# Optimization experiments

Hardware: AMD Instinct MI355X
Metric: run time of the kernel (lower is better)

Reference implementation:

```python
import jax, jax.numpy as jnp
import numpy as np

F_DIM = 256; L = 4; B = 1; H = 160; W = 160; FH = 1024; N = B * H * W

def _ln(x, w, b):
    mu = jnp.mean(x, -1, keepdims=True)
    var = jnp.mean(jnp.square(x - mu), -1, keepdims=True)
    return (x - mu) * jax.lax.rsqrt(var + 1e-5) * w + b

def _conv(x, w, b, groups=1, pad=0):
    y = jax.lax.conv_general_dilated(x, w, (1, 1), [(pad, pad), (pad, pad)],
                                     dimension_numbers=('NCHW', 'OIHW', 'NCHW'),
                                     feature_group_count=groups)
    return y + b[None, :, None, None]

def _wsilu(x):
    return jax.nn.sigmoid(4.0 * x) * x

def setup_inputs() -> dict:
    key = jax.random.key(0)
    ks = iter(jax.random.split(key, 40))
    nk = lambda: next(ks)
    s = 1.0 / np.sqrt(F_DIM).astype(np.float32)
    inp = {}
    inp['x'] = jax.random.normal(nk(), (B, 1, H, W), jnp.float32)
    inp['cin_w1'] = jax.random.normal(nk(), (F_DIM, 1, 1, 1), jnp.float32)
    inp['cin_b1'] = jnp.zeros((F_DIM,), jnp.float32)
    inp['cin_w2'] = jax.random.normal(nk(), (F_DIM, 1, 7, 7), jnp.float32) * 0.15
    inp['cin_b2'] = jnp.zeros((F_DIM,), jnp.float32)
    inp['ln0_w'] = jnp.ones((F_DIM,), jnp.float32); inp['ln0_b'] = jnp.zeros((F_DIM,), jnp.float32)
    inp['ln1_w'] = jnp.ones((L, F_DIM), jnp.float32); inp['ln1_b'] = jnp.zeros((L, F_DIM), jnp.float32)
    inp['ln2_w'] = jnp.ones((L, F_DIM), jnp.float32); inp['ln2_b'] = jnp.zeros((L, F_DIM), jnp.float32)
    for n in ['att_tmk', 'att_tmv', 'att_tmr', 'ffn_tmk', 'ffn_tmr']:
        inp[n] = jax.random.uniform(nk(), (L, F_DIM), jnp.float32)
    inp['att_tf'] = jax.random.normal(nk(), (L, F_DIM), jnp.float32) * 0.5
    # time_decay is stored as -exp(raw) by the module's loader
    inp['att_td'] = -jnp.exp(jax.random.normal(nk(), (L, F_DIM), jnp.float32) * 0.5)
    for n in ['att_kw', 'att_vw', 'att_rw', 'att_ow', 'ffn_rw']:
        inp[n] = jax.random.normal(nk(), (L, F_DIM, F_DIM), jnp.float32) * s
    inp['ffn_kw'] = jax.random.normal(nk(), (L, FH, F_DIM), jnp.float32) * s
    inp['ffn_vw'] = jax.random.normal(nk(), (L, F_DIM, FH), jnp.float32) * (1.0 / np.sqrt(FH).astype(np.float32))
    inp['spa_dw_w'] = jax.random.normal(nk(), (L, F_DIM, 1, 7, 7), jnp.float32) * 0.15
    inp['spa_dw_b'] = jnp.zeros((L, F_DIM), jnp.float32)
    inp['spa_pw_w'] = jax.random.normal(nk(), (L, F_DIM, F_DIM, 1, 1), jnp.float32) * s
    inp['spa_pw_b'] = jnp.zeros((L, F_DIM), jnp.float32)
    st = jnp.zeros((5 * L, N, F_DIM), jnp.float32)
    st = st.at[4::5].add(-1e30)  # pp slots start at -1e30 as in torch init
    inp['state0'] = st
    return inp

def reference(x, cin_w1, cin_b1, cin_w2, cin_b2, ln0_w, ln0_b, ln1_w, ln1_b,
              ln2_w, ln2_b, att_tmk, att_tmv, att_tmr, att_tf, att_td,
              att_kw, att_vw, att_rw, att_ow, ffn_tmk, ffn_tmr, ffn_kw,
              ffn_vw, ffn_rw, spa_dw_w, spa_dw_b, spa_pw_w, spa_pw_b, state0):
    # conv stem: 1x1 -> depthwise 7x7 -> WSiLU
    d = _conv(x, cin_w1, cin_b1)
    d = _wsilu(_conv(d, cin_w2, cin_b2, groups=F_DIM, pad=3))
    d = d.transpose(0, 2, 3, 1).reshape(N, F_DIM)  # 'b f h w -> (b h w) f'
    for i in range(L):
        if i == 0:
            d = _ln(d, ln0_w, ln0_b)
        # --- SA: single-step RWKV WKV ---
        xs = _ln(d, ln1_w[i], ln1_b[i])
        sp = state0[5 * i + 1]
        aa = state0[5 * i + 2]; bb = state0[5 * i + 3]; pp = state0[5 * i + 4]
        xk = xs * att_tmk[i] + sp * (1 - att_tmk[i])
        xv = xs * att_tmv[i] + sp * (1 - att_tmv[i])
        xr = xs * att_tmr[i] + sp * (1 - att_tmr[i])
        r = jax.nn.sigmoid(xr @ att_rw[i].T)
        k = xk @ att_kw[i].T
        v = xv @ att_vw[i].T
        ww = att_tf[i] + k
        p = jnp.maximum(pp, ww)
        e1 = jnp.exp(pp - p); e2 = jnp.exp(ww - p)
        wkv = (e1 * aa + e2 * v) / (e1 * bb + e2)
        d = d + (r * wkv) @ att_ow[i].T
        # --- FF: squared-relu channel mix ---
        xs = _ln(d, ln2_w[i], ln2_b[i])
        sp = state0[5 * i + 0]
        xk = xs * ffn_tmk[i] + sp * (1 - ffn_tmk[i])
        xr = xs * ffn_tmr[i] + sp * (1 - ffn_tmr[i])
        rr = jax.nn.sigmoid(xr @ ffn_rw[i].T)
        kk = jnp.square(jax.nn.relu(xk @ ffn_kw[i].T))
        d = d + rr * (kk @ ffn_vw[i].T)
        # --- spatial residual block ---
        img = d.reshape(B, H, W, F_DIM).transpose(0, 3, 1, 2)
        img = img + _conv(_conv(img, spa_dw_w[i], spa_dw_b[i], groups=F_DIM, pad=3),
                          spa_pw_w[i], spa_pw_b[i])
        d = img.transpose(0, 2, 3, 1).reshape(N, F_DIM)
    return d.reshape(B, H, W, F_DIM).transpose(0, 3, 1, 2)
```

## Files before the change

### kernel.cpp

```cpp
#include <hip/hip_runtime.h>
#include <hip/hip_bf16.h>
#include <cstdint>
#include <cstddef>

#define F_DIMC 256
#define FHC    1024
#define IMGH   160
#define IMGW   160
#define NTOK   25600
#define NLAY   4

using bf16 = __hip_bfloat16;
using f16  = _Float16;
typedef __attribute__((ext_vector_type(8))) short bf16x8;
typedef __attribute__((ext_vector_type(4))) float f32x4;

#define MFMA16(a, b, c) __builtin_amdgcn_mfma_f32_16x16x32_bf16((a), (b), (c), 0, 0, 0)

union H4 { f16 h[4]; uint2 u; };
union Pack4 { bf16 h[4]; uint2 u; };
union Pack8 { bf16 h[8]; bf16x8 v; };

__global__ void prep_k(const float* __restrict__ kw, const float* __restrict__ vw,
                       const float* __restrict__ rw, const float* __restrict__ tmk,
                       const float* __restrict__ tmv, const float* __restrict__ tmr,
                       const float* __restrict__ fkw, const float* __restrict__ ftmk,
                       const float* __restrict__ frw, const float* __restrict__ ftmr,
                       const float* __restrict__ ow, const float* __restrict__ pw,
                       const float* __restrict__ fvw, const float* __restrict__ dww,
                       bf16* __restrict__ Wcat, bf16* __restrict__ fkw2,
                       bf16* __restrict__ frw2, bf16* __restrict__ owb,
                       bf16* __restrict__ pwb, bf16* __restrict__ fvwb,
                       float* __restrict__ dwT)
{
    int z = blockIdx.y;
    int idx = blockIdx.x * 256 + threadIdx.x;
    if (z < 4) {
        int l = z;
        int c = idx & 511, cc = c & 255;
        bool hi2 = c >= 256;
        int r = idx >> 9;
        if (r < 768) {
            const float* W; const float* T; int rr = r;
            if (r < 256)      { W = kw; T = tmk; }
            else if (r < 512) { W = vw; T = tmv; rr = r - 256; }
            else              { W = rw; T = tmr; rr = r - 512; }
            float w = W[(size_t)l * 65536 + rr * 256 + cc];
            float t = T[l * 256 + cc];
            Wcat[(size_t)l * 768 * 512 + (size_t)r * 512 + c] = __float2bfloat16(w * (hi2 ? 1.f - t : t));
        } else if (r < 1792) {
            int rr = r - 768;
            float w = fkw[(size_t)l * 1024 * 256 + rr * 256 + cc];
            float t = ftmk[l * 256 + cc];
            fkw2[(size_t)l * 1024 * 512 + (size_t)rr * 512 + c] = __float2bfloat16(w * (hi2 ? 1.f - t : t));
        } else {
            int rr = r - 1792;
            float w = frw[(size_t)l * 65536 + rr * 256 + cc];
            float t = ftmr[l * 256 + cc];
            frw2[(size_t)l * 256 * 512 + (size_t)rr * 512 + c] = __float2bfloat16(w * (hi2 ? 1.f - t : t));
        }
    } else {
        int q = z - 4;
        if (q == 0)      { if (idx < 262144)  owb[idx]  = __float2bfloat16(ow[idx]); }
        else if (q == 1) { if (idx < 262144)  pwb[idx]  = __float2bfloat16(pw[idx]); }
        else if (q == 2) { if (idx < 1048576) fvwb[idx] = __float2bfloat16(fvw[idx]); }
        else {
            if (idx < 50176) {
                int f = idx & 255; int lt = idx >> 8; int t = lt % 49; int l = lt / 49;
                dwT[idx] = dww[((size_t)l * F_DIMC + f) * 49 + t];
            }
        }
    }
}

__global__ __launch_bounds__(256)
void stem2_k(const float* __restrict__ x, const float* __restrict__ w1,
             const float* __restrict__ b1, const float* __restrict__ w2,
             const float* __restrict__ b2, f16* __restrict__ d)
{
    __shared__ float wts[49][64];
    __shared__ float w1s[64], b1s[64], b2s[64];
    __shared__ float2 xp[7][22];
    const int tid = threadIdx.x;
    const int f0 = blockIdx.y * 64;
    const int y = blockIdx.x / 10;
    const int x0 = (blockIdx.x % 10) * 16;

    for (int idx = tid; idx < 49 * 64; idx += 256) {
        int t = idx >> 6, fl = idx & 63;
        wts[t][fl] = w2[(f0 + fl) * 49 + t];
    }
    if (tid < 64) {
        w1s[tid] = w1[f0 + tid];
        b1s[tid] = b1[f0 + tid];
        b2s[tid] = b2[f0 + tid];
    }
    for (int p = tid; p < 7 * 22; p += 256) {
        int py = p / 22, px = p % 22;
        int gy = y + py - 3, gx = x0 + px - 3;
        bool ok = (unsigned)gy < IMGH && (unsigned)gx < IMGW;
        xp[py][px] = ok ? make_float2(x[gy * IMGW + gx], 1.f) : make_float2(0.f, 0.f);
    }
    __syncthreads();

    const int fl = tid & 63;
    const int xbase = (tid >> 6) * 4;
    float acc[4] = {0.f, 0.f, 0.f, 0.f}, accw[4] = {0.f, 0.f, 0.f, 0.f};
    #pragma unroll
    for (int ky = 0; ky < 7; ++ky) {
        float2 row[10];
        #pragma unroll
        for (int q = 0; q < 10; ++q) row[q] = xp[ky][xbase + q];
        #pragma unroll
        for (int kx = 0; kx < 7; ++kx) {
            float w = wts[ky * 7 + kx][fl];
            #pragma unroll
            for (int j = 0; j < 4; ++j) {
                acc[j]  = fmaf(row[j + kx].x, w, acc[j]);
                accw[j] = fmaf(row[j + kx].y, w, accw[j]);
            }
        }
    }
    const float w1f = w1s[fl], b1f = b1s[fl], b2f = b2s[fl];
    #pragma unroll
    for (int j = 0; j < 4; ++j) {
        float u = fmaf(w1f, acc[j], fmaf(b1f, accw[j], b2f));
        int pix = y * IMGW + x0 + xbase + j;
        d[(size_t)pix * F_DIMC + f0 + fl] = (f16)(u / (1.f + __expf(-4.f * u)));
    }
}

__device__ __forceinline__ void wave_ln(float* x, const float* __restrict__ w,
                                        const float* __restrict__ b, int lane)
{
    float s = x[0] + x[1] + x[2] + x[3];
    #pragma unroll
    for (int m = 1; m < 64; m <<= 1) s += __shfl_xor(s, m, 64);
    float mu = s * 0.00390625f;
    float t0 = x[0] - mu, t1 = x[1] - mu, t2 = x[2] - mu, t3 = x[3] - mu;
    float v = t0 * t0 + t1 * t1 + t2 * t2 + t3 * t3;
    #pragma unroll
    for (int m = 1; m < 64; m <<= 1) v += __shfl_xor(v, m, 64);
    float inv = rsqrtf(v * 0.00390625f + 1e-5f);
    f32x4 wv = *(const f32x4*)(w + lane * 4);
    f32x4 bv = *(const f32x4*)(b + lane * 4);
    x[0] = t0 * inv * wv[0] + bv[0];
    x[1] = t1 * inv * wv[1] + bv[1];
    x[2] = t2 * inv * wv[2] + bv[2];
    x[3] = t3 * inv * wv[3] + bv[3];
}

__global__ __launch_bounds__(256)
void ln_first_k(f16* __restrict__ d, const float* __restrict__ ln0w,
                const float* __restrict__ ln0b, const float* __restrict__ l1w,
                const float* __restrict__ l1b, bf16* __restrict__ xs)
{
    const int lane = threadIdx.x & 63;
    const int n = blockIdx.x * 4 + (threadIdx.x >> 6);
    const int base = n * F_DIMC + lane * 4;
    H4 hv; hv.u = *(const uint2*)(d + base);
    float xo[4] = {(float)hv.h[0], (float)hv.h[1], (float)hv.h[2], (float)hv.h[3]};
    wave_ln(xo, ln0w, ln0b, lane);
    H4 o;
    #pragma unroll
    for (int j = 0; j < 4; ++j) o.h[j] = (f16)xo[j];
    *(uint2*)(d + base) = o.u;
    wave_ln(xo, l1w, l1b, lane);
    Pack4 p;
    #pragma unroll
    for (int j = 0; j < 4; ++j) p.h[j] = __float2bfloat16(xo[j]);
    *(uint2*)(xs + base) = p.u;
}

__device__ __forceinline__ void stage_swz16(const bf16* __restrict__ g, int lda,
                                            bf16* lds, int tid)
{
    #pragma unroll
    for (int s = 0; s < 8; ++s) {
        int chunk = s * 256 + tid;
        int row = chunk >> 4, c16 = chunk & 15;
        int gc = c16 ^ (row & 15);
        __builtin_amdgcn_global_load_lds(
            (const __attribute__((address_space(1))) void*)(g + (size_t)row * lda + gc * 8),
            (__attribute__((address_space(3))) void*)(lds + chunk * 8), 16, 0, 0);
    }
}
__device__ __forceinline__ void stage_f32_swz16(const float* __restrict__ g, int lda,
                                                bf16* lds, int tid)
{
    #pragma unroll
    for (int s = 0; s < 8; ++s) {
        int chunk = s * 256 + tid;
        int row = chunk >> 4, c16 = chunk & 15;
        int gc = c16 ^ (row & 15);
        const float* src = g + (size_t)row * lda + gc * 8;
        f32x4 a = *(const f32x4*)src;
        f32x4 b = *(const f32x4*)(src + 4);
        Pack8 p;
        #pragma unroll
        for (int j = 0; j < 4; ++j) p.h[j] = __float2bfloat16(a[j]);
        #pragma unroll
        for (int j = 0; j < 4; ++j) p.h[4 + j] = __float2bfloat16(b[j]);
        *(bf16x8*)(lds + chunk * 8) = p.v;
    }
}
__device__ __forceinline__ void stage_swz8(const bf16* __restrict__ g, int lda,
                                           bf16* lds, int tid, int nloads)
{
    #pragma unroll
    for (int s = 0; s < 8; ++s) {
        if (s >= nloads) break;
        int chunk = s * 256 + tid;
        int row = chunk >> 3, c = chunk & 7;
        int gc = c ^ (row & 7);
        __builtin_amdgcn_global_load_lds(
            (const __attribute__((address_space(1))) void*)(g + (size_t)row * lda + gc * 8),
            (__attribute__((address_space(3))) void*)(lds + chunk * 8), 16, 0, 0);
    }
}

template<int RB>
__device__ __forceinline__ bf16x8 frag_ld(const bf16* lds, int row, int cb)
{
    constexpr int M = (RB >= 256) ? 15 : (RB / 16 - 1);
    return *(const bf16x8*)((const char*)lds + row * RB + (cb ^ ((row & M) << 4)));
}

template<int EPI>
__global__ __launch_bounds__(256, 2)
void gemm128_k(const bf16* __restrict__ A1, const float* __restrict__ A2f,
               const bf16* __restrict__ Bw, int Nout,
               f16* __restrict__ Cf, bf16* __restrict__ Cb)
{
    __shared__ __align__(16) bf16 As[128 * 128];
    __shared__ __align__(16) bf16 Bs[128 * 128];
    const int tid = threadIdx.x, lane = tid & 63, wave = tid >> 6;
    const int wr = wave >> 1, wc = wave & 1;
    const int lr = lane & 15, hi = lane >> 4;
    const int m0 = blockIdx.x * 128, n0 = blockIdx.y * 128;

    f32x4 acc[4][4];
    #pragma unroll
    for (int m = 0; m < 4; ++m)
        #pragma unroll
        for (int n = 0; n < 4; ++n) acc[m][n] = (f32x4){0.f, 0.f, 0.f, 0.f};

    #pragma unroll
    for (int kt = 0; kt < 512; kt += 128) {
        if (kt < 256)
            stage_swz16(A1 + (size_t)m0 * 256 + kt, 256, As, tid);
        else
            stage_f32_swz16(A2f + (size_t)m0 * 256 + (kt - 256), 256, As, tid);
        stage_swz16(Bw + (size_t)n0 * 512 + kt, 512, Bs, tid);
        __syncthreads();
        #pragma unroll
        for (int ks = 0; ks < 4; ++ks) {
            int cb = ks * 64 + hi * 16;
            bf16x8 a[4], b[4];
            #pragma unroll
            for (int mf = 0; mf < 4; ++mf) a[mf] = frag_ld<256>(As, wr * 64 + mf * 16 + lr, cb);
            #pragma unroll
            for (int nf = 0; nf < 4; ++nf) b[nf] = frag_ld<256>(Bs, wc * 64 + nf * 16 + lr, cb);
            #pragma unroll
            for (int mf = 0; mf < 4; ++mf)
                #pragma unroll
                for (int nf = 0; nf < 4; ++nf)
                    acc[mf][nf] = MFMA16(a[mf], b[nf], acc[mf][nf]);
        }
        __syncthreads();
    }

    const int lr0 = hi * 4;
    #pragma unroll
    for (int mf = 0; mf < 4; ++mf)
        #pragma unroll
        for (int nf = 0; nf < 4; ++nf) {
            int col = n0 + wc * 64 + nf * 16 + lr;
            #pragma unroll
            for (int j = 0; j < 4; ++j) {
                int row = m0 + wr * 64 + mf * 16 + lr0 + j;
                size_t cidx = (size_t)row * Nout + col;
                float v = acc[mf][nf][j];
                if constexpr (EPI == 0) Cf[cidx] = (f16)v;
                else { float t = fmaxf(v, 0.f); Cb[cidx] = __float2bfloat16(t * t); }
            }
        }
}

__global__ __launch_bounds__(256, 2)
void gemmow_k(const f16* __restrict__ G, const float* __restrict__ aa,
              const float* __restrict__ bb, const float* __restrict__ pp,
              const float* __restrict__ tf, const bf16* __restrict__ W,
              f16* __restrict__ d, bf16* __restrict__ xs,
              const float* __restrict__ lnw, const float* __restrict__ lnb)
{
    __shared__ __align__(16) bf16 As[64 * 256];
    __shared__ __align__(16) bf16 Bs[256 * 64];
    __shared__ float2 lnp[64][4];
    const int tid = threadIdx.x, lane = tid & 63, wave = tid >> 6;
    const int lr = lane & 15, hi = lane >> 4;
    const int m0 = blockIdx.x * 64;

    stage_swz8(W, 256, Bs, tid, 8);

    #pragma unroll
    for (int rb = 0; rb < 4; ++rb) {
        int r = rb * 16 + (tid >> 4);
        int row = m0 + r;
        const f16* g = G + (size_t)row * 768;
        const size_t sb = (size_t)row * F_DIMC;
        #pragma unroll
        for (int j = 0; j < 4; ++j) {
            int c = (tid & 15) * 4 + j * 64;
            H4 k4; k4.u = *(const uint2*)(g + c);
            H4 v4; v4.u = *(const uint2*)(g + 256 + c);
            H4 r4; r4.u = *(const uint2*)(g + 512 + c);
            f32x4 a4 = *(const f32x4*)(aa + sb + c);
            f32x4 b4 = *(const f32x4*)(bb + sb + c);
            f32x4 p4 = *(const f32x4*)(pp + sb + c);
            f32x4 t4 = *(const f32x4*)(tf + c);
            Pack4 po;
            #pragma unroll
            for (int q = 0; q < 4; ++q) {
                float ww = t4[q] + (float)k4.h[q];
                float p = fmaxf(p4[q], ww);
                float e1 = __expf(p4[q] - p);
                float e2 = __expf(ww - p);
                float wkv = (e1 * a4[q] + e2 * (float)v4.h[q]) / (e1 * b4[q] + e2);
                float rs = 1.f / (1.f + __expf(-(float)r4.h[q]));
                po.h[q] = __float2bfloat16(rs * wkv);
            }
            int chunk = c >> 3;
            int off = (c & 4) ? 8 : 0;
            *(uint2*)((char*)As + r * 512 + ((chunk ^ (r & 15)) << 4) + off) = po.u;
        }
    }
    __syncthreads();

    f32x4 acc[4][4];
    #pragma unroll
    for (int m = 0; m < 4; ++m)
        #pragma unroll
        for (int n = 0; n < 4; ++n) acc[m][n] = (f32x4){0.f, 0.f, 0.f, 0.f};

    #pragma unroll
    for (int kt = 0; kt < 256; kt += 64) {
        if (kt > 0) {
            stage_swz8(W + kt, 256, Bs, tid, 8);
            __syncthreads();
        }
        #pragma unroll
        for (int ks = 0; ks < 2; ++ks) {
            int cbA = kt * 2 + ks * 64 + hi * 16;
            int cbB = ks * 64 + hi * 16;
            bf16x8 a[4], b[4];
            #pragma unroll
            for (int mf = 0; mf < 4; ++mf) a[mf] = frag_ld<512>(As, mf * 16 + lr, cbA);
            #pragma unroll
            for (int nf = 0; nf < 4; ++nf) b[nf] = frag_ld<128>(Bs, wave * 64 + nf * 16 + lr, cbB);
            #pragma unroll
            for (int mf = 0; mf < 4; ++mf)
                #pragma unroll
                for (int nf = 0; nf < 4; ++nf)
                    acc[mf][nf] = MFMA16(a[mf], b[nf], acc[mf][nf]);
        }
        __syncthreads();
    }

    const int lr0 = hi * 4;
    #pragma unroll
    for (int mf = 0; mf < 4; ++mf) {
        #pragma unroll
        for (int j = 0; j < 4; ++j) {
            int row = m0 + mf * 16 + lr0 + j;
            float s = 0.f, q = 0.f;
            #pragma unroll
            for (int nf = 0; nf < 4; ++nf) {
                int col = wave * 64 + nf * 16 + lr;
                size_t ci = (size_t)row * F_DIMC + col;
                float v = acc[mf][nf][j] + (float)d[ci];
                acc[mf][nf][j] = v;
                d[ci] = (f16)v;
                s += v; q += v * v;
            }
            #pragma unroll
            for (int m = 1; m < 16; m <<= 1) {
                s += __shfl_xor(s, m, 64);
                q += __shfl_xor(q, m, 64);
            }
            if (lr == 0) lnp[mf * 16 + lr0 + j][wave] = make_float2(s, q);
        }
    }
    __syncthreads();
    #pragma unroll
    for (int mf = 0; mf < 4; ++mf) {
        #pragma unroll
        for (int j = 0; j < 4; ++j) {
            int ri = mf * 16 + lr0 + j;
            float S = 0.f, Q = 0.f;
            #pragma unroll
            for (int w2 = 0; w2 < 4; ++w2) {
                float2 p = lnp[ri][w2];
                S += p.x; Q += p.y;
            }
            float mu = S * 0.00390625f;
            float var = Q * 0.00390625f - mu * mu;
            float inv = rsqrtf(var + 1e-5f);
            int row = m0 + ri;
            #pragma unroll
            for (int nf = 0; nf < 4; ++nf) {
                int col = wave * 64 + nf * 16 + lr;
                float v = (acc[mf][nf][j] - mu) * inv * lnw[col] + lnb[col];
                xs[(size_t)row * F_DIMC + col] = __float2bfloat16(v);
            }
        }
    }
}

template<bool DOLN>
__global__ __launch_bounds__(256, 2)
void gemmpw_k(const bf16* __restrict__ A, const bf16* __restrict__ W,
              f16* __restrict__ d, bf16* __restrict__ xs,
              const float* __restrict__ lnw, const float* __restrict__ lnb,
              const float* __restrict__ bias)
{
    __shared__ __align__(16) bf16 As[64 * 64];
    __shared__ __align__(16) bf16 Bs[256 * 64];
    __shared__ float2 lnp[64][4];
    const int tid = threadIdx.x, lane = tid & 63, wave = tid >> 6;
    const int lr = lane & 15, hi = lane >> 4;
    const int m0 = blockIdx.x * 64;

    f32x4 acc[4][4];
    #pragma unroll
    for (int m = 0; m < 4; ++m)
        #pragma unroll
        for (int n = 0; n < 4; ++n) acc[m][n] = (f32x4){0.f, 0.f, 0.f, 0.f};

    #pragma unroll
    for (int kt = 0; kt < 256; kt += 64) {
        stage_swz8(A + (size_t)m0 * 256 + kt, 256, As, tid, 2);
        stage_swz8(W + kt, 256, Bs, tid, 8);
        __syncthreads();
        #pragma unroll
        for (int ks = 0; ks < 2; ++ks) {
            int cb = ks * 64 + hi * 16;
            bf16x8 a[4], b[4];
            #pragma unroll
            for (int mf = 0; mf < 4; ++mf) a[mf] = frag_ld<128>(As, mf * 16 + lr, cb);
            #pragma unroll
            for (int nf = 0; nf < 4; ++nf) b[nf] = frag_ld<128>(Bs, wave * 64 + nf * 16 + lr, cb);
            #pragma unroll
            for (int mf = 0; mf < 4; ++mf)
                #pragma unroll
                for (int nf = 0; nf < 4; ++nf)
                    acc[mf][nf] = MFMA16(a[mf], b[nf], acc[mf][nf]);
        }
        __syncthreads();
    }

    const int lr0 = hi * 4;
    #pragma unroll
    for (int mf = 0; mf < 4; ++mf) {
        #pragma unroll
        for (int j = 0; j < 4; ++j) {
            int row = m0 + mf * 16 + lr0 + j;
            float s = 0.f, q = 0.f;
            #pragma unroll
            for (int nf = 0; nf < 4; ++nf) {
                int col = wave * 64 + nf * 16 + lr;
                size_t ci = (size_t)row * F_DIMC + col;
                float v = acc[mf][nf][j] + (float)d[ci] + bias[col];
                acc[mf][nf][j] = v;
                d[ci] = (f16)v;
                s += v; q += v * v;
            }
            if constexpr (DOLN) {
                #pragma unroll
                for (int m = 1; m < 16; m <<= 1) {
                    s += __shfl_xor(s, m, 64);
                    q += __shfl_xor(q, m, 64);
                }
                if (lr == 0) lnp[mf * 16 + lr0 + j][wave] = make_float2(s, q);
            }
        }
    }
    if constexpr (DOLN) {
        __syncthreads();
        #pragma unroll
        for (int mf = 0; mf < 4; ++mf) {
            #pragma unroll
            for (int j = 0; j < 4; ++j) {
                int ri = mf * 16 + lr0 + j;
                float S = 0.f, Q = 0.f;
                #pragma unroll
                for (int w2 = 0; w2 < 4; ++w2) {
                    float2 p = lnp[ri][w2];
                    S += p.x; Q += p.y;
                }
                float mu = S * 0.00390625f;
                float var = Q * 0.00390625f - mu * mu;
                float inv = rsqrtf(var + 1e-5f);
                int row = m0 + ri;
                #pragma unroll
                for (int nf = 0; nf < 4; ++nf) {
                    int col = wave * 64 + nf * 16 + lr;
                    float v = (acc[mf][nf][j] - mu) * inv * lnw[col] + lnb[col];
                    xs[(size_t)row * F_DIMC + col] = __float2bfloat16(v);
                }
            }
        }
    }
}

__global__ __launch_bounds__(256, 2)
void fvwrr_k(const bf16* __restrict__ kkb, const bf16* __restrict__ fvw,
             const bf16* __restrict__ xs, const float* __restrict__ spf,
             const bf16* __restrict__ frw2, f16* __restrict__ d)
{
    __shared__ __align__(16) bf16 As[128 * 128];
    __shared__ __align__(16) bf16 Bs[128 * 128];
    const int tid = threadIdx.x, lane = tid & 63, wave = tid >> 6;
    const int wr = wave >> 1, wc = wave & 1;
    const int lr = lane & 15, hi = lane >> 4;
    const int m0 = blockIdx.x * 128, n0 = blockIdx.y * 128;

    f32x4 arr[4][4], am[4][4];
    #pragma unroll
    for (int m = 0; m < 4; ++m)
        #pragma unroll
        for (int n = 0; n < 4; ++n) {
            arr[m][n] = (f32x4){0.f, 0.f, 0.f, 0.f};
            am[m][n]  = (f32x4){0.f, 0.f, 0.f, 0.f};
        }

    #pragma unroll
    for (int kt = 0; kt < 512; kt += 128) {
        if (kt < 256)
            stage_swz16(xs + (size_t)m0 * 256 + kt, 256, As, tid);
        else
            stage_f32_swz16(spf + (size_t)m0 * 256 + (kt - 256), 256, As, tid);
        stage_swz16(frw2 + (size_t)n0 * 512 + kt, 512, Bs, tid);
        __syncthreads();
        #pragma unroll
        for (int ks = 0; ks < 4; ++ks) {
            int cb = ks * 64 + hi * 16;
            bf16x8 a[4], b[4];
            #pragma unroll
            for (int mf = 0; mf < 4; ++mf) a[mf] = frag_ld<256>(As, wr * 64 + mf * 16 + lr, cb);
            #pragma unroll
            for (int nf = 0; nf < 4; ++nf) b[nf] = frag_ld<256>(Bs, wc * 64 + nf * 16 + lr, cb);
            #pragma unroll
            for (int mf = 0; mf < 4; ++mf)
                #pragma unroll
                for (int nf = 0; nf < 4; ++nf)
                    arr[mf][nf] = MFMA16(a[mf], b[nf], arr[mf][nf]);
        }
        __syncthreads();
    }
    #pragma unroll
    for (int kt = 0; kt < 1024; kt += 128) {
        stage_swz16(kkb + (size_t)m0 * 1024 + kt, 1024, As, tid);
        stage_swz16(fvw + (size_t)n0 * 1024 + kt, 1024, Bs, tid);
        __syncthreads();
        #pragma unroll
        for (int ks = 0; ks < 4; ++ks) {
            int cb = ks * 64 + hi * 16;
            bf16x8 a[4], b[4];
            #pragma unroll
            for (int mf = 0; mf < 4; ++mf) a[mf] = frag_ld<256>(As, wr * 64 + mf * 16 + lr, cb);
            #pragma unroll
            for (int nf = 0; nf < 4; ++nf) b[nf] = frag_ld<256>(Bs, wc * 64 + nf * 16 + lr, cb);
            #pragma unroll
            for (int mf = 0; mf < 4; ++mf)
                #pragma unroll
                for (int nf = 0; nf < 4; ++nf)
                    am[mf][nf] = MFMA16(a[mf], b[nf], am[mf][nf]);
        }
        __syncthreads();
    }

    const int lr0 = hi * 4;
    #pragma unroll
    for (int mf = 0; mf < 4; ++mf)
        #pragma unroll
        for (int nf = 0; nf < 4; ++nf) {
            int col = n0 + wc * 64 + nf * 16 + lr;
            #pragma unroll
            for (int j = 0; j < 4; ++j) {
                int row = m0 + wr * 64 + mf * 16 + lr0 + j;
                size_t cidx = (size_t)row * F_DIMC + col;
                float rr = 1.f / (1.f + __expf(-arr[mf][nf][j]));
                d[cidx] = (f16)((float)d[cidx] + rr * am[mf][nf][j]);
            }
        }
}

__global__ __launch_bounds__(256)
void dwconv2_k(const f16* __restrict__ d, const float* __restrict__ wT,
               const float* __restrict__ bias, bf16* __restrict__ out)
{
    __shared__ float patch[196][64];
    __shared__ float wt[49][64];
    const int lane = threadIdx.x;
    const int ty = threadIdx.y;
    const int f0 = blockIdx.z * 64;
    const int w0 = blockIdx.x * 8, h0 = blockIdx.y * 8;

    for (int t = ty; t < 49; t += 4) wt[t][lane] = wT[t * F_DIMC + f0 + lane];
    for (int p = ty; p < 196; p += 4) {
        int py = p / 14, px = p % 14;
        int gy = h0 + py - 3, gx = w0 + px - 3;
        float v = 0.f;
        if ((unsigned)gy < IMGH && (unsigned)gx < IMGW)
            v = (float)d[(size_t)(gy * IMGW + gx) * F_DIMC + f0 + lane];
        patch[p][lane] = v;
    }
    __syncthreads();

    const float b = bias[f0 + lane];
    #pragma unroll
    for (int rr = 0; rr < 2; ++rr) {
        int ry = ty * 2 + rr;
        float acc8[8];
        #pragma unroll
        for (int px = 0; px < 8; ++px) acc8[px] = b;
        #pragma unroll
        for (int ky = 0; ky < 7; ++ky) {
            float rowv[14];
            #pragma unroll
            for (int c = 0; c < 14; ++c) rowv[c] = patch[(ry + ky) * 14 + c][lane];
            #pragma unroll
            for (int kx = 0; kx < 7; ++kx) {
                float w = wt[ky * 7 + kx][lane];
                #pragma unroll
                for (int px = 0; px < 8; ++px)
                    acc8[px] = fmaf(rowv[px + kx], w, acc8[px]);
            }
        }
        #pragma unroll
        for (int px = 0; px < 8; ++px)
            out[(size_t)((h0 + ry) * IMGW + (w0 + px)) * F_DIMC + f0 + lane] = __float2bfloat16(acc8[px]);
    }
}

__global__ __launch_bounds__(256)
void transpose_out_k(const f16* __restrict__ d, float* __restrict__ out)
{
    __shared__ float tile[32][33];
    const int n0 = blockIdx.x * 32, f0 = blockIdx.y * 32;
    const int tx = threadIdx.x, ty = threadIdx.y;
    for (int r = ty; r < 32; r += 8) tile[r][tx] = (float)d[(size_t)(n0 + r) * F_DIMC + f0 + tx];
    __syncthreads();
    for (int r = ty; r < 32; r += 8) out[(size_t)(f0 + r) * NTOK + n0 + tx] = tile[tx][r];
}

extern "C" void kernel_launch(void* const* d_in, const int* in_sizes, int n_in,
                              void* d_out, int out_size, void* d_ws, size_t ws_size,
                              hipStream_t stream)
{
    if (n_in < 30) return;
    const float* x        = (const float*)d_in[0];
    const float* cin_w1   = (const float*)d_in[1];
    const float* cin_b1   = (const float*)d_in[2];
    const float* cin_w2   = (const float*)d_in[3];
    const float* cin_b2   = (const float*)d_in[4];
    const float* ln0_w    = (const float*)d_in[5];
    const float* ln0_b    = (const float*)d_in[6];
    const float* ln1_w    = (const float*)d_in[7];
    const float* ln1_b    = (const float*)d_in[8];
    const float* ln2_w    = (const float*)d_in[9];
    const float* ln2_b    = (const float*)d_in[10];
    const float* att_tmk  = (const float*)d_in[11];
    const float* att_tmv  = (const float*)d_in[12];
    const float* att_tmr  = (const float*)d_in[13];
    const float* ffn_tmk  = (const float*)d_in[14];
    const float* ffn_tmr  = (const float*)d_in[15];
    const float* att_tf   = (const float*)d_in[16];
    const float* att_kw   = (const float*)d_in[18];
    const float* att_vw   = (const float*)d_in[19];
    const float* att_rw   = (const float*)d_in[20];
    const float* att_ow   = (const float*)d_in[21];
    const float* ffn_rw   = (const float*)d_in[22];
    const float* ffn_kw   = (const float*)d_in[23];
    const float* ffn_vw   = (const float*)d_in[24];
    const float* spa_dw_w = (const float*)d_in[25];
    const float* spa_dw_b = (const float*)d_in[26];
    const float* spa_pw_w = (const float*)d_in[27];
    const float* spa_pw_b = (const float*)d_in[28];
    const float* state0   = (const float*)d_in[29];
    float* out = (float*)d_out;

    const size_t NF = (size_t)NTOK * F_DIMC;
    char* wsp = (char*)d_ws;
    size_t off = 0;
    auto alloc = [&](size_t bytes) -> void* {
        void* p = wsp + off;
        off += (bytes + 255) & ~(size_t)255;
        return p;
    };
    f16*   d_buf = (f16*)alloc(NF * 2);
    bf16*  xs    = (bf16*)alloc(NF * 2);
    f16*   G     = (f16*)alloc((size_t)NTOK * 768 * 2);
    bf16*  ab    = (bf16*)alloc(NF * 2);
    bf16*  kkb   = (bf16*)alloc((size_t)NTOK * FHC * 2);
    bf16*  Wcat  = (bf16*)alloc((size_t)NLAY * 768 * 512 * 2);
    bf16*  fkw2  = (bf16*)alloc((size_t)NLAY * 1024 * 512 * 2);
    bf16*  frw2  = (bf16*)alloc((size_t)NLAY * 256 * 512 * 2);
    bf16*  owb   = (bf16*)alloc((size_t)NLAY * 65536 * 2);
    bf16*  pwb   = (bf16*)alloc((size_t)NLAY * 65536 * 2);
    bf16*  fvwb  = (bf16*)alloc((size_t)NLAY * 262144 * 2);
    float* dwT   = (float*)alloc((size_t)NLAY * 49 * F_DIMC * 4);
    if (off > ws_size) return;

    prep_k<<<dim3(4096, 8), dim3(256), 0, stream>>>(
        att_kw, att_vw, att_rw, att_tmk, att_tmv, att_tmr,
        ffn_kw, ffn_tmk, ffn_rw, ffn_tmr,
        att_ow, spa_pw_w, ffn_vw, spa_dw_w,
        Wcat, fkw2, frw2, owb, pwb, fvwb, dwT);

    stem2_k<<<dim3(IMGH * 10, 4), dim3(256), 0, stream>>>(x, cin_w1, cin_b1, cin_w2, cin_b2, d_buf);
    ln_first_k<<<dim3(NTOK / 4), dim3(256), 0, stream>>>(d_buf, ln0_w, ln0_b, ln1_w, ln1_b, xs);

    for (int i = 0; i < NLAY; ++i) {
        const float* sp_ff = state0 + (size_t)(5 * i + 0) * NF;
        const float* sp_at = state0 + (size_t)(5 * i + 1) * NF;
        const float* aa    = state0 + (size_t)(5 * i + 2) * NF;
        const float* bb    = state0 + (size_t)(5 * i + 3) * NF;
        const float* pp    = state0 + (size_t)(5 * i + 4) * NF;
        const float* tf    = att_tf + i * F_DIMC;
        const bf16* Wcat_i = Wcat + (size_t)i * 768 * 512;
        const bf16* fkw2_i = fkw2 + (size_t)i * 1024 * 512;
        const bf16* frw2_i = frw2 + (size_t)i * 256 * 512;
        const bf16* ow_i   = owb  + (size_t)i * 65536;
        const bf16* pw_i   = pwb  + (size_t)i * 65536;
        const bf16* fvw_i  = fvwb + (size_t)i * 262144;
        const float* dwT_i = dwT + (size_t)i * 49 * F_DIMC;
        const float* dwb_i = spa_dw_b + i * F_DIMC;
        const float* pwbias_i = spa_pw_b + i * F_DIMC;

        gemm128_k<0><<<dim3(NTOK / 128, 6), dim3(256), 0, stream>>>(
            xs, sp_at, Wcat_i, 768, G, nullptr);
        gemmow_k<<<dim3(NTOK / 64), dim3(256), 0, stream>>>(
            G, aa, bb, pp, tf, ow_i, d_buf, xs, ln2_w + i * F_DIMC, ln2_b + i * F_DIMC);
        gemm128_k<2><<<dim3(NTOK / 128, 8), dim3(256), 0, stream>>>(
            xs, sp_ff, fkw2_i, 1024, nullptr, kkb);
        fvwrr_k<<<dim3(NTOK / 128, 2), dim3(256), 0, stream>>>(
            kkb, fvw_i, xs, sp_ff, frw2_i, d_buf);
        dwconv2_k<<<dim3(IMGW / 8, IMGH / 8, 4), dim3(64, 4), 0, stream>>>(d_buf, dwT_i, dwb_i, ab);
        if (i < NLAY - 1)
            gemmpw_k<true><<<dim3(NTOK / 64), dim3(256), 0, stream>>>(
                ab, pw_i, d_buf, xs, ln1_w + (i + 1) * F_DIMC, ln1_b + (i + 1) * F_DIMC, pwbias_i);
        else
            gemmpw_k<false><<<dim3(NTOK / 64), dim3(256), 0, stream>>>(
                ab, pw_i, d_buf, xs, nullptr, nullptr, pwbias_i);
    }

    transpose_out_k<<<dim3(NTOK / 32, F_DIMC / 32), dim3(32, 8), 0, stream>>>(d_buf, out);
}
```

Baseline: 2.013 ms.

## Pack LN output and bf16 shift-state into a combined A buffer; use row-band GEMMs

```diff
diff --git a/kernel.cpp b/kernel.cpp
--- a/kernel.cpp
+++ b/kernel.cpp
@@ -19,7 +19,6 @@
 
 union H4 { f16 h[4]; uint2 u; };
 union Pack4 { bf16 h[4]; uint2 u; };
-union Pack8 { bf16 h[8]; bf16x8 v; };
 
 __global__ void prep_k(const float* __restrict__ kw, const float* __restrict__ vw,
                        const float* __restrict__ rw, const float* __restrict__ tmk,
@@ -153,7 +152,8 @@
 __global__ __launch_bounds__(256)
 void ln_first_k(f16* __restrict__ d, const float* __restrict__ ln0w,
                 const float* __restrict__ ln0b, const float* __restrict__ l1w,
-                const float* __restrict__ l1b, bf16* __restrict__ xs)
+                const float* __restrict__ l1b, const float* __restrict__ spf,
+                bf16* __restrict__ xsp)
 {
     const int lane = threadIdx.x & 63;
     const int n = blockIdx.x * 4 + (threadIdx.x >> 6);
@@ -169,39 +169,26 @@
     Pack4 p;
     #pragma unroll
     for (int j = 0; j < 4; ++j) p.h[j] = __float2bfloat16(xo[j]);
-    *(uint2*)(xs + base) = p.u;
-}
-
-__device__ __forceinline__ void stage_swz16(const bf16* __restrict__ g, int lda,
-                                            bf16* lds, int tid)
-{
-    #pragma unroll
-    for (int s = 0; s < 8; ++s) {
+    *(uint2*)(xsp + (size_t)n * 512 + lane * 4) = p.u;
+    f32x4 sv = *(const f32x4*)(spf + base);
+    Pack4 ps;
+    #pragma unroll
+    for (int j = 0; j < 4; ++j) ps.h[j] = __float2bfloat16(sv[j]);
+    *(uint2*)(xsp + (size_t)n * 512 + 256 + lane * 4) = ps.u;
+}
+
+template<int ROWS>
+__device__ __forceinline__ void stage_swz_rows(const bf16* __restrict__ g, int lda,
+                                               bf16* lds, int tid)
+{
+    #pragma unroll
+    for (int s = 0; s < ROWS / 16; ++s) {
         int chunk = s * 256 + tid;
         int row = chunk >> 4, c16 = chunk & 15;
         int gc = c16 ^ (row & 15);
         __builtin_amdgcn_global_load_lds(
             (const __attribute__((address_space(1))) void*)(g + (size_t)row * lda + gc * 8),
             (__attribute__((address_space(3))) void*)(lds + chunk * 8), 16, 0, 0);
-    }
-}
-__device__ __forceinline__ void stage_f32_swz16(const float* __restrict__ g, int lda,
-                                                bf16* lds, int tid)
-{
-    #pragma unroll
-    for (int s = 0; s < 8; ++s) {
-        int chunk = s * 256 + tid;
-        int row = chunk >> 4, c16 = chunk & 15;
-        int gc = c16 ^ (row & 15);
-        const float* src = g + (size_t)row * lda + gc * 8;
-        f32x4 a = *(const f32x4*)src;
-        f32x4 b = *(const f32x4*)(src + 4);
-        Pack8 p;
-        #pragma unroll
-        for (int j = 0; j < 4; ++j) p.h[j] = __float2bfloat16(a[j]);
-        #pragma unroll
-        for (int j = 0; j < 4; ++j) p.h[4 + j] = __float2bfloat16(b[j]);
-        *(bf16x8*)(lds + chunk * 8) = p.v;
     }
 }
 __device__ __forceinline__ void stage_swz8(const bf16* __restrict__ g, int lda,
@@ -226,73 +213,73 @@
     return *(const bf16x8*)((const char*)lds + row * RB + (cb ^ ((row & M) << 4)));
 }
 
-template<int EPI>
-__global__ __launch_bounds__(256, 2)
-void gemm128_k(const bf16* __restrict__ A1, const float* __restrict__ A2f,
-               const bf16* __restrict__ Bw, int Nout,
-               f16* __restrict__ Cf, bf16* __restrict__ Cb)
-{
-    __shared__ __align__(16) bf16 As[128 * 128];
+template<int NT, int EPI>
+__global__ __launch_bounds__(256, 3)
+void bandgemm_k(const bf16* __restrict__ xsp, const bf16* __restrict__ Bw,
+                f16* __restrict__ Cf, bf16* __restrict__ Cb)
+{
+    __shared__ __align__(16) bf16 As[64 * 128];
     __shared__ __align__(16) bf16 Bs[128 * 128];
     const int tid = threadIdx.x, lane = tid & 63, wave = tid >> 6;
     const int wr = wave >> 1, wc = wave & 1;
     const int lr = lane & 15, hi = lane >> 4;
-    const int m0 = blockIdx.x * 128, n0 = blockIdx.y * 128;
-
-    f32x4 acc[4][4];
-    #pragma unroll
-    for (int m = 0; m < 4; ++m)
-        #pragma unroll
-        for (int n = 0; n < 4; ++n) acc[m][n] = (f32x4){0.f, 0.f, 0.f, 0.f};
-
-    #pragma unroll
-    for (int kt = 0; kt < 512; kt += 128) {
-        if (kt < 256)
-            stage_swz16(A1 + (size_t)m0 * 256 + kt, 256, As, tid);
-        else
-            stage_f32_swz16(A2f + (size_t)m0 * 256 + (kt - 256), 256, As, tid);
-        stage_swz16(Bw + (size_t)n0 * 512 + kt, 512, Bs, tid);
-        __syncthreads();
-        #pragma unroll
-        for (int ks = 0; ks < 4; ++ks) {
-            int cb = ks * 64 + hi * 16;
-            bf16x8 a[4], b[4];
-            #pragma unroll
-            for (int mf = 0; mf < 4; ++mf) a[mf] = frag_ld<256>(As, wr * 64 + mf * 16 + lr, cb);
-            #pragma unroll
-            for (int nf = 0; nf < 4; ++nf) b[nf] = frag_ld<256>(Bs, wc * 64 + nf * 16 + lr, cb);
-            #pragma unroll
-            for (int mf = 0; mf < 4; ++mf)
-                #pragma unroll
-                for (int nf = 0; nf < 4; ++nf)
-                    acc[mf][nf] = MFMA16(a[mf], b[nf], acc[mf][nf]);
-        }
-        __syncthreads();
-    }
-
-    const int lr0 = hi * 4;
-    #pragma unroll
-    for (int mf = 0; mf < 4; ++mf)
-        #pragma unroll
-        for (int nf = 0; nf < 4; ++nf) {
-            int col = n0 + wc * 64 + nf * 16 + lr;
-            #pragma unroll
-            for (int j = 0; j < 4; ++j) {
-                int row = m0 + wr * 64 + mf * 16 + lr0 + j;
-                size_t cidx = (size_t)row * Nout + col;
-                float v = acc[mf][nf][j];
-                if constexpr (EPI == 0) Cf[cidx] = (f16)v;
-                else { float t = fmaxf(v, 0.f); Cb[cidx] = __float2bfloat16(t * t); }
-            }
-        }
+    const int m0 = blockIdx.x * 64;
+    const int Nout = NT * 128;
+
+    for (int nt = 0; nt < NT; ++nt) {
+        f32x4 acc[2][4];
+        #pragma unroll
+        for (int m = 0; m < 2; ++m)
+            #pragma unroll
+            for (int n = 0; n < 4; ++n) acc[m][n] = (f32x4){0.f, 0.f, 0.f, 0.f};
+
+        #pragma unroll
+        for (int kt = 0; kt < 512; kt += 128) {
+            stage_swz_rows<64>(xsp + (size_t)m0 * 512 + kt, 512, As, tid);
+            stage_swz_rows<128>(Bw + (size_t)(nt * 128) * 512 + kt, 512, Bs, tid);
+            __syncthreads();
+            #pragma unroll
+            for (int ks = 0; ks < 4; ++ks) {
+                int cb = ks * 64 + hi * 16;
+                bf16x8 a[2], b[4];
+                #pragma unroll
+                for (int mf = 0; mf < 2; ++mf) a[mf] = frag_ld<256>(As, wr * 32 + mf * 16 + lr, cb);
+                #pragma unroll
+                for (int nf = 0; nf < 4; ++nf) b[nf] = frag_ld<256>(Bs, wc * 64 + nf * 16 + lr, cb);
+                #pragma unroll
+                for (int mf = 0; mf < 2; ++mf)
+                    #pragma unroll
+                    for (int nf = 0; nf < 4; ++nf)
+                        acc[mf][nf] = MFMA16(a[mf], b[nf], acc[mf][nf]);
+            }
+            __syncthreads();
+        }
+
+        const int lr0 = hi * 4;
+        #pragma unroll
+        for (int mf = 0; mf < 2; ++mf)
+            #pragma unroll
+            for (int nf = 0; nf < 4; ++nf) {
+                int col = nt * 128 + wc * 64 + nf * 16 + lr;
+                #pragma unroll
+                for (int j = 0; j < 4; ++j) {
+                    int row = m0 + wr * 32 + mf * 16 + lr0 + j;
+                    size_t cidx = (size_t)row * Nout + col;
+                    float v = acc[mf][nf][j];
+                    if constexpr (EPI == 0) Cf[cidx] = (f16)v;
+                    else { float t = fmaxf(v, 0.f); Cb[cidx] = __float2bfloat16(t * t); }
+                }
+            }
+    }
 }
 
 __global__ __launch_bounds__(256, 2)
 void gemmow_k(const f16* __restrict__ G, const float* __restrict__ aa,
               const float* __restrict__ bb, const float* __restrict__ pp,
               const float* __restrict__ tf, const bf16* __restrict__ W,
-              f16* __restrict__ d, bf16* __restrict__ xs,
-              const float* __restrict__ lnw, const float* __restrict__ lnb)
+              f16* __restrict__ d, bf16* __restrict__ xsp,
+              const float* __restrict__ lnw, const float* __restrict__ lnb,
+              const float* __restrict__ spf)
 {
     __shared__ __align__(16) bf16 As[64 * 256];
     __shared__ __align__(16) bf16 Bs[256 * 64];
@@ -411,18 +398,28 @@
             for (int nf = 0; nf < 4; ++nf) {
                 int col = wave * 64 + nf * 16 + lr;
                 float v = (acc[mf][nf][j] - mu) * inv * lnw[col] + lnb[col];
-                xs[(size_t)row * F_DIMC + col] = __float2bfloat16(v);
-            }
-        }
+                xsp[(size_t)row * 512 + col] = __float2bfloat16(v);
+            }
+        }
+    }
+    #pragma unroll
+    for (int it = 0; it < 16; ++it) {
+        int e = it * 1024 + tid * 4;
+        int r = e >> 8, c = e & 255;
+        f32x4 sv = *(const f32x4*)(spf + (size_t)(m0 + r) * F_DIMC + c);
+        Pack4 ps;
+        #pragma unroll
+        for (int j = 0; j < 4; ++j) ps.h[j] = __float2bfloat16(sv[j]);
+        *(uint2*)(xsp + (size_t)(m0 + r) * 512 + 256 + c) = ps.u;
     }
 }
 
 template<bool DOLN>
 __global__ __launch_bounds__(256, 2)
 void gemmpw_k(const bf16* __restrict__ A, const bf16* __restrict__ W,
-              f16* __restrict__ d, bf16* __restrict__ xs,
+              f16* __restrict__ d, bf16* __restrict__ xsp,
               const float* __restrict__ lnw, const float* __restrict__ lnb,
-              const float* __restrict__ bias)
+              const float* __restrict__ bias, const float* __restrict__ spf)
 {
     __shared__ __align__(16) bf16 As[64 * 64];
     __shared__ __align__(16) bf16 Bs[256 * 64];
@@ -506,17 +503,27 @@
                 for (int nf = 0; nf < 4; ++nf) {
                     int col = wave * 64 + nf * 16 + lr;
                     float v = (acc[mf][nf][j] - mu) * inv * lnw[col] + lnb[col];
-                    xs[(size_t)row * F_DIMC + col] = __float2bfloat16(v);
+                    xsp[(size_t)row * 512 + col] = __float2bfloat16(v);
                 }
             }
+        }
+        #pragma unroll
+        for (int it = 0; it < 16; ++it) {
+            int e = it * 1024 + tid * 4;
+            int r = e >> 8, c = e & 255;
+            f32x4 sv = *(const f32x4*)(spf + (size_t)(m0 + r) * F_DIMC + c);
+            Pack4 ps;
+            #pragma unroll
+            for (int j = 0; j < 4; ++j) ps.h[j] = __float2bfloat16(sv[j]);
+            *(uint2*)(xsp + (size_t)(m0 + r) * 512 + 256 + c) = ps.u;
         }
     }
 }
 
 __global__ __launch_bounds__(256, 2)
 void fvwrr_k(const bf16* __restrict__ kkb, const bf16* __restrict__ fvw,
-             const bf16* __restrict__ xs, const float* __restrict__ spf,
-             const bf16* __restrict__ frw2, f16* __restrict__ d)
+             const bf16* __restrict__ xsp, const bf16* __restrict__ frw2,
+             f16* __restrict__ d)
 {
     __shared__ __align__(16) bf16 As[128 * 128];
     __shared__ __align__(16) bf16 Bs[128 * 128];
@@ -536,11 +543,8 @@
 
     #pragma unroll
     for (int kt = 0; kt < 512; kt += 128) {
-        if (kt < 256)
-            stage_swz16(xs + (size_t)m0 * 256 + kt, 256, As, tid);
-        else
-            stage_f32_swz16(spf + (size_t)m0 * 256 + (kt - 256), 256, As, tid);
-        stage_swz16(frw2 + (size_t)n0 * 512 + kt, 512, Bs, tid);
+        stage_swz_rows<128>(xsp + (size_t)m0 * 512 + kt, 512, As, tid);
+        stage_swz_rows<128>(frw2 + (size_t)n0 * 512 + kt, 512, Bs, tid);
         __syncthreads();
         #pragma unroll
         for (int ks = 0; ks < 4; ++ks) {
@@ -560,8 +564,8 @@
     }
     #pragma unroll
     for (int kt = 0; kt < 1024; kt += 128) {
-        stage_swz16(kkb + (size_t)m0 * 1024 + kt, 1024, As, tid);
-        stage_swz16(fvw + (size_t)n0 * 1024 + kt, 1024, Bs, tid);
+        stage_swz_rows<128>(kkb + (size_t)m0 * 1024 + kt, 1024, As, tid);
+        stage_swz_rows<128>(fvw + (size_t)n0 * 1024 + kt, 1024, Bs, tid);
         __syncthreads();
         #pragma unroll
         for (int ks = 0; ks < 4; ++ks) {
@@ -700,7 +704,7 @@
         return p;
     };
     f16*   d_buf = (f16*)alloc(NF * 2);
-    bf16*  xs    = (bf16*)alloc(NF * 2);
+    bf16*  xsp   = (bf16*)alloc((size_t)NTOK * 512 * 2);
     f16*   G     = (f16*)alloc((size_t)NTOK * 768 * 2);
     bf16*  ab    = (bf16*)alloc(NF * 2);
     bf16*  kkb   = (bf16*)alloc((size_t)NTOK * FHC * 2);
@@ -720,11 +724,11 @@
         Wcat, fkw2, frw2, owb, pwb, fvwb, dwT);
 
     stem2_k<<<dim3(IMGH * 10, 4), dim3(256), 0, stream>>>(x, cin_w1, cin_b1, cin_w2, cin_b2, d_buf);
-    ln_first_k<<<dim3(NTOK / 4), dim3(256), 0, stream>>>(d_buf, ln0_w, ln0_b, ln1_w, ln1_b, xs);
+    ln_first_k<<<dim3(NTOK / 4), dim3(256), 0, stream>>>(
+        d_buf, ln0_w, ln0_b, ln1_w, ln1_b, state0 + 1 * NF, xsp);
 
     for (int i = 0; i < NLAY; ++i) {
         const float* sp_ff = state0 + (size_t)(5 * i + 0) * NF;
-        const float* sp_at = state0 + (size_t)(5 * i + 1) * NF;
         const float* aa    = state0 + (size_t)(5 * i + 2) * NF;
         const float* bb    = state0 + (size_t)(5 * i + 3) * NF;
         const float* pp    = state0 + (size_t)(5 * i + 4) * NF;
@@ -739,21 +743,20 @@
         const float* dwb_i = spa_dw_b + i * F_DIMC;
         const float* pwbias_i = spa_pw_b + i * F_DIMC;
 
-        gemm128_k<0><<<dim3(NTOK / 128, 6), dim3(256), 0, stream>>>(
-            xs, sp_at, Wcat_i, 768, G, nullptr);
+        bandgemm_k<6, 0><<<dim3(NTOK / 64), dim3(256), 0, stream>>>(xsp, Wcat_i, G, nullptr);
         gemmow_k<<<dim3(NTOK / 64), dim3(256), 0, stream>>>(
-            G, aa, bb, pp, tf, ow_i, d_buf, xs, ln2_w + i * F_DIMC, ln2_b + i * F_DIMC);
-        gemm128_k<2><<<dim3(NTOK / 128, 8), dim3(256), 0, stream>>>(
-            xs, sp_ff, fkw2_i, 1024, nullptr, kkb);
-        fvwrr_k<<<dim3(NTOK / 128, 2), dim3(256), 0, stream>>>(
-            kkb, fvw_i, xs, sp_ff, frw2_i, d_buf);
+            G, aa, bb, pp, tf, ow_i, d_buf, xsp,
+            ln2_w + i * F_DIMC, ln2_b + i * F_DIMC, sp_ff);
+        bandgemm_k<8, 2><<<dim3(NTOK / 64), dim3(256), 0, stream>>>(xsp, fkw2_i, nullptr, kkb);
+        fvwrr_k<<<dim3(NTOK / 128, 2), dim3(256), 0, stream>>>(kkb, fvw_i, xsp, frw2_i, d_buf);
         dwconv2_k<<<dim3(IMGW / 8, IMGH / 8, 4), dim3(64, 4), 0, stream>>>(d_buf, dwT_i, dwb_i, ab);
         if (i < NLAY - 1)
             gemmpw_k<true><<<dim3(NTOK / 64), dim3(256), 0, stream>>>(
-                ab, pw_i, d_buf, xs, ln1_w + (i + 1) * F_DIMC, ln1_b + (i + 1) * F_DIMC, pwbias_i);
+                ab, pw_i, d_buf, xsp, ln1_w + (i + 1) * F_DIMC, ln1_b + (i + 1) * F_DIMC,
+                pwbias_i, state0 + (size_t)(5 * (i + 1) + 1) * NF);
         else
             gemmpw_k<false><<<dim3(NTOK / 64), dim3(256), 0, stream>>>(
-                ab, pw_i, d_buf, xs, nullptr, nullptr, pwbias_i);
+                ab, pw_i, d_buf, xsp, nullptr, nullptr, pwbias_i, nullptr);
     }
 
     transpose_out_k<<<dim3(NTOK / 32, F_DIMC / 32), dim3(32, 8), 0, stream>>>(d_buf, out);
```

New measurement: 2.127 ms. 1.06x slower.
